# Optimization experiments

Measured on AMD Instinct MI355X. Metric: run time of the kernel, lower is better.

Reference implementation:

```python
import jax, jax.numpy as jnp
import numpy as np

D_MODEL = 1024
NUM_HEADS = 16
D_K = D_MODEL // NUM_HEADS


def setup_inputs() -> dict:
    key = jax.random.key(0)
    ks = jax.random.split(key, 10)
    s = 1.0 / np.sqrt(D_MODEL)  # ~ torch Linear init scale
    inp = {
        "x": jax.random.normal(ks[0], (2, 2048, D_MODEL), dtype=jnp.float32),
        "Wq": jax.random.uniform(ks[1], (D_MODEL, D_MODEL), jnp.float32, -s, s),
        "bq": jax.random.uniform(ks[2], (D_MODEL,), jnp.float32, -s, s),
        "Wk": jax.random.uniform(ks[3], (D_MODEL, D_MODEL), jnp.float32, -s, s),
        "bk": jax.random.uniform(ks[4], (D_MODEL,), jnp.float32, -s, s),
        "Wv": jax.random.uniform(ks[5], (D_MODEL, D_MODEL), jnp.float32, -s, s),
        "bv": jax.random.uniform(ks[6], (D_MODEL,), jnp.float32, -s, s),
        "Wo": jax.random.uniform(ks[7], (D_MODEL, D_MODEL), jnp.float32, -s, s),
        "bo": jax.random.uniform(ks[8], (D_MODEL,), jnp.float32, -s, s),
        "ln_gamma": jnp.ones((D_MODEL,), jnp.float32),
        "ln_beta": jnp.zeros((D_MODEL,), jnp.float32),
    }
    return inp


def reference(x, Wq, bq, Wk, bk, Wv, bv, Wo, bo, ln_gamma, ln_beta):
    B, S, D = x.shape
    residual = x
    # LayerNorm (eps=1e-5 as torch default)
    mu = jnp.mean(x, axis=-1, keepdims=True)
    var = jnp.mean(jnp.square(x - mu), axis=-1, keepdims=True)
    xn = (x - mu) * jax.lax.rsqrt(var + 1e-5) * ln_gamma + ln_beta
    # QKV projections (torch Linear: y = x @ W^T + b) -> (B, H, S, d_k)
    def proj(W, b):
        return (xn @ W.T + b).reshape(B, S, NUM_HEADS, D_K).transpose(0, 2, 1, 3)
    Q, K, V = proj(Wq, bq), proj(Wk, bk), proj(Wv, bv)
    scores = jnp.einsum("bhqd,bhkd->bhqk", Q, K) / np.sqrt(D_K).astype(np.float32)
    attn = jax.nn.softmax(scores, axis=-1)  # (B, H, S, S); dropout is no-op (eval)
    context = jnp.einsum("bhqk,bhkd->bhqd", attn, V)
    context = context.transpose(0, 2, 1, 3).reshape(B, S, D)
    out = context @ Wo.T + bo
    return out + residual, attn.mean(axis=1)
```

## Files before the change

kernel.cpp:

```cpp
#include <hip/hip_runtime.h>
#include <stdint.h>
#include <stddef.h>

#define DEV static __device__ __forceinline__

typedef float f32x4 __attribute__((ext_vector_type(4)));
typedef float f32x16 __attribute__((ext_vector_type(16)));
typedef unsigned u32x4 __attribute__((ext_vector_type(4)));
typedef __bf16 bf16x8 __attribute__((ext_vector_type(8)));

DEV short f2bf(float f) {
  union { float f; unsigned u; } a; a.f = f;
  unsigned r = a.u + 0x7fffu + ((a.u >> 16) & 1u);
  return (short)(r >> 16);
}

DEV void gld_lds16(const void* g, void* lds) {
  __builtin_amdgcn_global_load_lds(
      (__attribute__((address_space(1))) void*)(void*)g,
      (__attribute__((address_space(3))) void*)lds, 16, 0, 0);
}

DEV f32x4 MFMA(bf16x8 a, bf16x8 b, f32x4 c) {
  return __builtin_amdgcn_mfma_f32_16x16x32_bf16(a, b, c, 0, 0, 0);
}
DEV f32x16 MFMA32(bf16x8 a, bf16x8 b, f32x16 c) {
  return __builtin_amdgcn_mfma_f32_32x32x16_bf16(a, b, c, 0, 0, 0);
}

DEV float ex2(float x) { return __builtin_amdgcn_exp2f(x); }

DEV unsigned cvtpk(float lo, float hi) {
  unsigned r;
  asm("v_cvt_pk_bf16_f32 %0, %1, %2" : "=v"(r) : "v"(lo), "v"(hi));
  return r;
}

DEV float xhalf_sum(float v) {
  float a = v, b = v;
  asm volatile("v_permlane32_swap_b32 %0, %1" : "+v"(a), "+v"(b));
  return a + b;
}

#define LOG2E 1.4426950408889634f


__global__ __launch_bounds__(256) void k_cvtw_ln(
    const float* __restrict__ w0, const float* __restrict__ w1,
    const float* __restrict__ w2, const float* __restrict__ w3,
    short* __restrict__ dst, const float* __restrict__ x,
    const float* __restrict__ g, const float* __restrict__ be,
    short* __restrict__ xn) {
  __shared__ float ps[4], pss[4];
  if (blockIdx.x < 4096) {
    int i = blockIdx.x * 256 + threadIdx.x;
    int sel = i >> 18;
    const float* src = sel == 0 ? w0 : sel == 1 ? w1 : sel == 2 ? w2 : w3;
    int off = (i & 0x3ffff) * 4;
    float4 v = *(const float4*)(src + off);
    short4 o4; o4.x = f2bf(v.x); o4.y = f2bf(v.y); o4.z = f2bf(v.z); o4.w = f2bf(v.w);
    *(short4*)(dst + (size_t)i * 4) = o4;
  } else {
    int row = blockIdx.x - 4096;
    int t = threadIdx.x;
    const float4* xr = (const float4*)(x + (size_t)row * 1024);
    float4 v = xr[t];
    float s = v.x + v.y + v.z + v.w;
    float ss = v.x * v.x + v.y * v.y + v.z * v.z + v.w * v.w;
#pragma unroll
    for (int o = 32; o; o >>= 1) { s += __shfl_down(s, o); ss += __shfl_down(ss, o); }
    int w = t >> 6, lane = t & 63;
    if (lane == 0) { ps[w] = s; pss[w] = ss; }
    __syncthreads();
    float st = ps[0] + ps[1] + ps[2] + ps[3];
    float sst = pss[0] + pss[1] + pss[2] + pss[3];
    float mean = st * (1.0f / 1024.0f);
    float var = sst * (1.0f / 1024.0f) - mean * mean;
    float rstd = rsqrtf(var + 1e-5f);
    float4 gv = ((const float4*)g)[t];
    float4 bv = ((const float4*)be)[t];
    short4 o4;
    o4.x = f2bf((v.x - mean) * rstd * gv.x + bv.x);
    o4.y = f2bf((v.y - mean) * rstd * gv.y + bv.y);
    o4.z = f2bf((v.z - mean) * rstd * gv.z + bv.z);
    o4.w = f2bf((v.w - mean) * rstd * gv.w + bv.w);
    ((short4*)(xn + (size_t)row * 1024))[t] = o4;
  }
}

__global__ __launch_bounds__(256) void k_gemm_qkv(
    const short* __restrict__ xn, const short* __restrict__ wbf,
    const float* __restrict__ bq, const float* __restrict__ bk,
    const float* __restrict__ bv, short* __restrict__ q_ws,
    short* __restrict__ k_ws, short* __restrict__ v_ws) {
  __shared__ __align__(16) short at[128 * 32];
  __shared__ __align__(16) short bt[128 * 32];
  int t = threadIdx.x, lane = t & 63, w = t >> 6;
  int wr = w >> 1, wc = w & 1;
  int z = blockIdx.z;
  int row0 = blockIdx.y * 128, col0 = blockIdx.x * 128;
  const short* A = xn + (size_t)row0 * 1024;
  const short* Bw = wbf + (size_t)z * (1024 * 1024) + (size_t)col0 * 1024;
  f32x4 acc[4][4];
#pragma unroll
  for (int m = 0; m < 4; m++)
#pragma unroll
    for (int n = 0; n < 4; n++) acc[m][n] = (f32x4)0.0f;

  for (int k0 = 0; k0 < 1024; k0 += 32) {
#pragma unroll
    for (int i = 0; i < 2; i++) {
      int c = t + i * 256;
      int r = c >> 2, cc = (c & 3) * 8;
      gld_lds16(A + (size_t)r * 1024 + k0 + cc, &at[c * 8]);
      gld_lds16(Bw + (size_t)r * 1024 + k0 + cc, &bt[c * 8]);
    }
    __syncthreads();
    bf16x8 af[4], bfr[4];
#pragma unroll
    for (int m = 0; m < 4; m++)
      af[m] = *(const bf16x8*)&at[(wr * 64 + m * 16 + (lane & 15)) * 32 + (lane >> 4) * 8];
#pragma unroll
    for (int n = 0; n < 4; n++)
      bfr[n] = *(const bf16x8*)&bt[(wc * 64 + n * 16 + (lane & 15)) * 32 + (lane >> 4) * 8];
#pragma unroll
    for (int m = 0; m < 4; m++)
#pragma unroll
      for (int n = 0; n < 4; n++) acc[m][n] = MFMA(af[m], bfr[n], acc[m][n]);
    __syncthreads();
  }
  const float* bias = z == 0 ? bq : z == 1 ? bk : bv;
  short* dst = z == 0 ? q_ws : z == 1 ? k_ws : v_ws;
  float scal = z == 0 ? (0.125f * LOG2E) : 1.0f;
#pragma unroll
  for (int m = 0; m < 4; m++)
#pragma unroll
    for (int n = 0; n < 4; n++)
#pragma unroll
      for (int r = 0; r < 4; r++) {
        int grow = row0 + wr * 64 + m * 16 + (lane >> 4) * 4 + r;
        int gcol = col0 + wc * 64 + n * 16 + (lane & 15);
        float val = (acc[m][n][r] + bias[gcol]) * scal;
        int bb = grow >> 11, s = grow & 2047, h = gcol >> 6, d = gcol & 63;
        dst[(((size_t)bb * 16 + h) * 2048 + s) * 64 + d] = f2bf(val);
      }
}

__global__ __launch_bounds__(256) void k_trv(const short* __restrict__ v_ws,
                                             short* __restrict__ vt_ws) {
  __shared__ short tile[64][65];
  int bh = blockIdx.y, s0 = blockIdx.x * 64;
  const short* src = v_ws + ((size_t)bh * 2048 + s0) * 64;
  int t = threadIdx.x;
#pragma unroll
  for (int i = 0; i < 4; i++) {
    int c = t + i * 256;
    int r = c >> 4, d4 = (c & 15) * 4;
    short4 v4 = *(const short4*)&src[r * 64 + d4];
    tile[d4 + 0][r] = v4.x; tile[d4 + 1][r] = v4.y;
    tile[d4 + 2][r] = v4.z; tile[d4 + 3][r] = v4.w;
  }
  __syncthreads();
#pragma unroll
  for (int i = 0; i < 4; i++) {
    int c = t + i * 256;
    int d = c >> 4, r4 = (c & 15) * 4;
    short4 o4;
    o4.x = tile[d][r4 + 0]; o4.y = tile[d][r4 + 1];
    o4.z = tile[d][r4 + 2]; o4.w = tile[d][r4 + 3];
    *(short4*)&vt_ws[((size_t)bh * 64 + d) * 2048 + s0 + r4] = o4;
  }
}

__global__ __launch_bounds__(256, 2) void k_attn1(
    const short* __restrict__ q_ws, const short* __restrict__ k_ws,
    const short* __restrict__ vt_ws, short* __restrict__ o_ws,
    float* __restrict__ l_ws) {
  __shared__ __align__(16) short k_lds[4][64 * 64];
  __shared__ __align__(16) short vt_lds[5][64 * 64];
  int t = threadIdx.x, lane = t & 63, w = t >> 6;
  int hi = lane >> 5, l31 = lane & 31;
  int flat = blockIdx.x + 16 * blockIdx.y + 256 * blockIdx.z;
  int mm = (flat & 7) * 64 + (flat >> 3);
  int qt = mm & 15, hd = (mm >> 4) & 15, b = mm >> 8;
  int bh = b * 16 + hd;
  int q0 = qt * 128;
  const short* qb = q_ws + (size_t)bh * (2048 * 64);
  const short* kb = k_ws + (size_t)bh * (2048 * 64);
  const short* vtb = vt_ws + (size_t)bh * (64 * 2048);
  int qg = q0 + w * 32 + l31;

  bf16x8 qf[4];
#pragma unroll
  for (int d4 = 0; d4 < 4; d4++)
    qf[d4] = *(const bf16x8*)&qb[(size_t)qg * 64 + d4 * 16 + hi * 8];
  asm volatile("s_waitcnt vmcnt(0)" ::: "memory");

  const short *kp0, *kp1, *vp0, *vp1;
  {
    int c = t, r = c >> 3, j = (c & 7) ^ (r & 7);
    kp0 = kb + (size_t)r * 64 + j * 8;
    vp0 = vtb + (size_t)r * 2048 + j * 8;
  }
  {
    int c = t + 256, r = c >> 3, j = (c & 7) ^ (r & 7);
    kp1 = kb + (size_t)r * 64 + j * 8;
    vp1 = vtb + (size_t)r * 2048 + j * 8;
  }

  int koff[8];
#pragma unroll
  for (int d4 = 0; d4 < 4; d4++) {
    int row0 = l31, row1 = 32 + l31;
    koff[2 * d4]     = row0 * 64 + (((d4 * 2 + hi) ^ (row0 & 7)) * 8);
    koff[2 * d4 + 1] = row1 * 64 + (((d4 * 2 + hi) ^ (row1 & 7)) * 8);
  }

#define STG(tl_)                                                         \
  {                                                                      \
    gld_lds16(kp0 + (size_t)(tl_) * 4096, &k_lds[(tl_) & 3][t * 8]);     \
    gld_lds16(kp1 + (size_t)(tl_) * 4096, &k_lds[(tl_) & 3][(t + 256) * 8]); \
    gld_lds16(vp0 + (size_t)(tl_) * 64, &vt_lds[(tl_) % 5][t * 8]);      \
    gld_lds16(vp1 + (size_t)(tl_) * 64, &vt_lds[(tl_) % 5][(t + 256) * 8]); \
  }

  STG(0);
  STG(1);

  f32x16 Oacc[2];
#pragma unroll
  for (int i = 0; i < 16; i++) { Oacc[0][i] = 0.0f; Oacc[1][i] = 0.0f; }
  float lrun = 0.0f;
  bf16x8 pb[4];

  for (int it = 0; it < 32; ++it) {
    int tn = it + 2 <= 31 ? it + 2 : 31;
    STG(tn);
    asm volatile("s_waitcnt vmcnt(8)" ::: "memory");
    __builtin_amdgcn_s_barrier();

    const short* kl = k_lds[it & 3];
    const short* vl = vt_lds[(it + 4) % 5];

    bf16x8 kfr[8], vfr[8];
#pragma unroll
    for (int i = 0; i < 8; i++) kfr[i] = *(const bf16x8*)&kl[koff[i]];
#pragma unroll
    for (int i = 0; i < 8; i++) vfr[i] = *(const bf16x8*)&vl[koff[i]];

    __builtin_amdgcn_s_setprio(1);
    f32x16 S0 = (f32x16)0.0f, S1 = (f32x16)0.0f;
#pragma unroll
    for (int d4 = 0; d4 < 4; d4++) {
      S0 = MFMA32(kfr[2 * d4], qf[d4], S0);
      S1 = MFMA32(kfr[2 * d4 + 1], qf[d4], S1);
    }
    if (it) {
#pragma unroll
      for (int ks = 0; ks < 4; ks++) {
        Oacc[0] = MFMA32(vfr[2 * ks], pb[ks], Oacc[0]);
        Oacc[1] = MFMA32(vfr[2 * ks + 1], pb[ks], Oacc[1]);
      }
    }
    __builtin_amdgcn_s_setprio(0);

    float rs0 = 0.0f, rs1 = 0.0f;
#pragma unroll
    for (int i = 0; i < 16; i++) {
      float p0 = ex2(S0[i]);
      float p1 = ex2(S1[i]);
      S0[i] = p0; S1[i] = p1;
      rs0 += p0; rs1 += p1;
    }
    lrun += xhalf_sum(rs0 + rs1);

#pragma unroll
    for (int ks = 0; ks < 4; ks++) {
      unsigned wA, wB, wC, wD;
      if (ks == 0) {
        wA = cvtpk(S0[0], S0[1]);  wB = cvtpk(S0[2], S0[3]);
        wC = cvtpk(S0[4], S0[5]);  wD = cvtpk(S0[6], S0[7]);
      } else if (ks == 1) {
        wA = cvtpk(S0[8], S0[9]);  wB = cvtpk(S0[10], S0[11]);
        wC = cvtpk(S0[12], S0[13]); wD = cvtpk(S0[14], S0[15]);
      } else if (ks == 2) {
        wA = cvtpk(S1[0], S1[1]);  wB = cvtpk(S1[2], S1[3]);
        wC = cvtpk(S1[4], S1[5]);  wD = cvtpk(S1[6], S1[7]);
      } else {
        wA = cvtpk(S1[8], S1[9]);  wB = cvtpk(S1[10], S1[11]);
        wC = cvtpk(S1[12], S1[13]); wD = cvtpk(S1[14], S1[15]);
      }
      asm volatile("v_permlane32_swap_b32 %0, %1" : "+v"(wA), "+v"(wC));
      asm volatile("v_permlane32_swap_b32 %0, %1" : "+v"(wB), "+v"(wD));
      u32x4 uu; uu.x = wA; uu.y = wB; uu.z = wC; uu.w = wD;
      pb[ks] = __builtin_bit_cast(bf16x8, uu);
    }
  }
  asm volatile("s_waitcnt vmcnt(0)" ::: "memory");
  __builtin_amdgcn_s_barrier();

  {
    const short* vl = vt_lds[1];
    __builtin_amdgcn_s_setprio(1);
#pragma unroll
    for (int ks = 0; ks < 4; ks++) {
      Oacc[0] = MFMA32(*(const bf16x8*)&vl[koff[2 * ks]], pb[ks], Oacc[0]);
      Oacc[1] = MFMA32(*(const bf16x8*)&vl[koff[2 * ks + 1]], pb[ks], Oacc[1]);
    }
    __builtin_amdgcn_s_setprio(0);
  }

  float rl = 1.0f / lrun;
  if (lane < 32) {
    l_ws[bh * 2048 + qg] = rl;
  }
#pragma unroll
  for (int dt = 0; dt < 2; dt++)
#pragma unroll
    for (int g = 0; g < 4; g++) {
      short4 o4;
      o4.x = f2bf(Oacc[dt][g * 4 + 0] * rl);
      o4.y = f2bf(Oacc[dt][g * 4 + 1] * rl);
      o4.z = f2bf(Oacc[dt][g * 4 + 2] * rl);
      o4.w = f2bf(Oacc[dt][g * 4 + 3] * rl);
      int d = dt * 32 + g * 8 + hi * 4;
      *(short4*)&o_ws[((size_t)(b * 2048 + qg)) * 1024 + hd * 64 + d] = o4;
    }
}

__global__ __launch_bounds__(256, 3) void k_attn2(
    const short* __restrict__ q_ws, const short* __restrict__ k_ws,
    const float* __restrict__ l_ws, float* __restrict__ out1) {
  __shared__ __align__(16) short k_lds2[3][128 * 64];
  __shared__ __align__(16) float l_lds[3][64];
  int t = threadIdx.x, lane = t & 63, w = t >> 6;
  int flat = blockIdx.x + 16 * blockIdx.y + 512 * blockIdx.z;
  int mm = (flat & 7) * 128 + (flat >> 3);
  int q0 = (mm & 31) * 64, k2 = ((mm >> 5) & 15) * 128, b = mm >> 9;

  f32x4 pacc[8];
#pragma unroll
  for (int n = 0; n < 8; n++) pacc[n] = (f32x4)0.0f;

  int qrow = q0 + w * 16 + (lane & 15);
  size_t qoff0 = (size_t)qrow * 64 + (lane >> 4) * 8;
  const short* qb0 = q_ws + (size_t)(b * 16) * (2048 * 64);

#define STAGE2(hh)                                                               \
  {                                                                              \
    int bh_ = b * 16 + (hh);                                                     \
    const short* kb_ = k_ws + (size_t)bh_ * (2048 * 64);                         \
    _Pragma("unroll")                                                            \
    for (int i = 0; i < 4; i++) {                                                \
      int c = t + i * 256;                                                       \
      int r = c >> 3, j = (c & 7) ^ (r & 7);                                     \
      gld_lds16(kb_ + (size_t)(k2 + r) * 64 + j * 8, &k_lds2[(hh) % 3][c * 8]);  \
    }                                                                            \
    int cc = w * 4 + (t & 63);                                                   \
    if ((t & 63) < 4) {                                                          \
      gld_lds16(&l_ws[(size_t)bh_ * 2048 + q0 + cc * 4], &l_lds[(hh) % 3][cc * 4]); \
    }                                                                            \
  }

  STAGE2(0);
  for (int h = 0; h < 16; ++h) {
    bf16x8 qf0 = *(const bf16x8*)&qb0[(size_t)h * (2048 * 64) + qoff0];
    bf16x8 qf1 = *(const bf16x8*)&qb0[(size_t)h * (2048 * 64) + qoff0 + 32];
    int hn = h < 15 ? h + 1 : 15;
    STAGE2(hn);
    asm volatile("s_waitcnt vmcnt(5)" ::: "memory");
    __builtin_amdgcn_s_barrier();

    const short* kl = k_lds2[h % 3];
    f32x4 sc[8];
#pragma unroll
    for (int n = 0; n < 8; n++) sc[n] = (f32x4)0.0f;
#pragma unroll
    for (int kf = 0; kf < 2; kf++)
#pragma unroll
      for (int n = 0; n < 8; n++) {
        int row = n * 16 + (lane & 15);
        bf16x8 kfr = *(const bf16x8*)&kl[row * 64 + (((kf * 4 + (lane >> 4)) ^ (row & 7)) * 8)];
        sc[n] = MFMA(kf == 0 ? qf0 : qf1, kfr, sc[n]);
      }
    f32x4 lh = *(const f32x4*)&l_lds[h % 3][w * 16 + (lane >> 4) * 4];
#pragma unroll
    for (int n = 0; n < 8; n++)
#pragma unroll
      for (int r = 0; r < 4; r++)
        pacc[n][r] += ex2(sc[n][r]) * lh[r];
  }

#pragma unroll
  for (int n = 0; n < 8; n++)
#pragma unroll
    for (int r = 0; r < 4; r++) {
      int q = q0 + w * 16 + (lane >> 4) * 4 + r;
      int k = k2 + n * 16 + (lane & 15);
      out1[((size_t)b * 2048 + q) * 2048 + k] = pacc[n][r] * 0.0625f;
    }
}

__global__ __launch_bounds__(256) void k_gemm_out(
    const short* __restrict__ o_ws, const short* __restrict__ wo_bf,
    const float* __restrict__ bo, const float* __restrict__ x,
    float* __restrict__ out0) {
  __shared__ __align__(16) short at[128 * 32];
  __shared__ __align__(16) short bt[128 * 32];
  int t = threadIdx.x, lane = t & 63, w = t >> 6;
  int wr = w >> 1, wc = w & 1;
  int row0 = blockIdx.y * 128, col0 = blockIdx.x * 128;
  const short* A = o_ws + (size_t)row0 * 1024;
  const short* Bw = wo_bf + (size_t)col0 * 1024;
  f32x4 acc[4][4];
#pragma unroll
  for (int m = 0; m < 4; m++)
#pragma unroll
    for (int n = 0; n < 4; n++) acc[m][n] = (f32x4)0.0f;

  for (int k0 = 0; k0 < 1024; k0 += 32) {
#pragma unroll
    for (int i = 0; i < 2; i++) {
      int c = t + i * 256;
      int r = c >> 2, cc = (c & 3) * 8;
      gld_lds16(A + (size_t)r * 1024 + k0 + cc, &at[c * 8]);
      gld_lds16(Bw + (size_t)r * 1024 + k0 + cc, &bt[c * 8]);
    }
    __syncthreads();
    bf16x8 af[4], bfr[4];
#pragma unroll
    for (int m = 0; m < 4; m++)
      af[m] = *(const bf16x8*)&at[(wr * 64 + m * 16 + (lane & 15)) * 32 + (lane >> 4) * 8];
#pragma unroll
    for (int n = 0; n < 4; n++)
      bfr[n] = *(const bf16x8*)&bt[(wc * 64 + n * 16 + (lane & 15)) * 32 + (lane >> 4) * 8];
#pragma unroll
    for (int m = 0; m < 4; m++)
#pragma unroll
      for (int n = 0; n < 4; n++) acc[m][n] = MFMA(af[m], bfr[n], acc[m][n]);
    __syncthreads();
  }
#pragma unroll
  for (int m = 0; m < 4; m++)
#pragma unroll
    for (int n = 0; n < 4; n++)
#pragma unroll
      for (int r = 0; r < 4; r++) {
        int grow = row0 + wr * 64 + m * 16 + (lane >> 4) * 4 + r;
        int gcol = col0 + wc * 64 + n * 16 + (lane & 15);
        float val = acc[m][n][r] + bo[gcol] + x[(size_t)grow * 1024 + gcol];
        out0[(size_t)grow * 1024 + gcol] = val;
      }
}

extern "C" void kernel_launch(void* const* d_in, const int* in_sizes, int n_in,
                              void* d_out, int out_size, void* d_ws, size_t ws_size,
                              hipStream_t stream) {
  (void)in_sizes; (void)n_in; (void)out_size; (void)ws_size;
  const float* x   = (const float*)d_in[0];
  const float* Wq  = (const float*)d_in[1];
  const float* bq  = (const float*)d_in[2];
  const float* Wk  = (const float*)d_in[3];
  const float* bk  = (const float*)d_in[4];
  const float* Wv  = (const float*)d_in[5];
  const float* bv  = (const float*)d_in[6];
  const float* Wo  = (const float*)d_in[7];
  const float* bo  = (const float*)d_in[8];
  const float* lng = (const float*)d_in[9];
  const float* lnb = (const float*)d_in[10];
  float* out0 = (float*)d_out;
  float* out1 = out0 + (size_t)2 * 2048 * 1024;

  char* ws = (char*)d_ws;
  short* xn    = (short*)(ws);
  short* q_ws  = (short*)(ws + 8388608);
  short* k_ws  = (short*)(ws + 16777216);
  short* o_ws  = (short*)(ws + 25165824);
  short* vt_ws = (short*)(ws + 33554432);
  short* wbf   = (short*)(ws + 41943040);
  float* l_ws  = (float*)(ws + 50331648);

  k_cvtw_ln<<<8192, 256, 0, stream>>>(Wq, Wk, Wv, Wo, wbf, x, lng, lnb, xn);
  k_gemm_qkv<<<dim3(8, 32, 3), 256, 0, stream>>>(xn, wbf, bq, bk, bv, q_ws, k_ws, o_ws);
  k_trv<<<dim3(32, 32), 256, 0, stream>>>(o_ws, vt_ws);
  k_attn1<<<dim3(16, 16, 2), 256, 0, stream>>>(q_ws, k_ws, vt_ws, o_ws, l_ws);
  k_attn2<<<dim3(16, 32, 2), 256, 0, stream>>>(q_ws, k_ws, l_ws, out1);
  k_gemm_out<<<dim3(8, 32), 256, 0, stream>>>(o_ws, wbf + (size_t)3 * 1024 * 1024, bo, x, out0);
}
```

Measured before the change: 161.8 us.

## Merge attention-map and output-projection kernels into one heterogeneous launch

Combines k_attn2 (averaged attention probabilities) and k_gemm_out (output projection plus residual) into a single kernel, k_tail, that dispatches on blockIdx: the first 256 blocks run the GEMM and the remaining 1024 run the attention-map pass. This removes one launch and the serialization gap between the two independent kernels, letting their work overlap on the GPU. In exchange the shared LDS allocation becomes the larger of the two and the launch_bounds occupancy hint of 3 is dropped, which may lower occupancy for the attention-map blocks.

Result: no change. 161.0 us (-0.5%).

```diff
diff --git a/kernel.cpp b/kernel.cpp
--- a/kernel.cpp
+++ b/kernel.cpp
@@ -328,129 +328,133 @@
     }
 }
 
-__global__ __launch_bounds__(256, 3) void k_attn2(
+__global__ __launch_bounds__(256) void k_tail(
     const short* __restrict__ q_ws, const short* __restrict__ k_ws,
-    const float* __restrict__ l_ws, float* __restrict__ out1) {
-  __shared__ __align__(16) short k_lds2[3][128 * 64];
-  __shared__ __align__(16) float l_lds[3][64];
-  int t = threadIdx.x, lane = t & 63, w = t >> 6;
-  int flat = blockIdx.x + 16 * blockIdx.y + 512 * blockIdx.z;
-  int mm = (flat & 7) * 128 + (flat >> 3);
-  int q0 = (mm & 31) * 64, k2 = ((mm >> 5) & 15) * 128, b = mm >> 9;
-
-  f32x4 pacc[8];
-#pragma unroll
-  for (int n = 0; n < 8; n++) pacc[n] = (f32x4)0.0f;
-
-  int qrow = q0 + w * 16 + (lane & 15);
-  size_t qoff0 = (size_t)qrow * 64 + (lane >> 4) * 8;
-  const short* qb0 = q_ws + (size_t)(b * 16) * (2048 * 64);
-
-#define STAGE2(hh)                                                               \
-  {                                                                              \
-    int bh_ = b * 16 + (hh);                                                     \
-    const short* kb_ = k_ws + (size_t)bh_ * (2048 * 64);                         \
-    _Pragma("unroll")                                                            \
-    for (int i = 0; i < 4; i++) {                                                \
-      int c = t + i * 256;                                                       \
-      int r = c >> 3, j = (c & 7) ^ (r & 7);                                     \
-      gld_lds16(kb_ + (size_t)(k2 + r) * 64 + j * 8, &k_lds2[(hh) % 3][c * 8]);  \
-    }                                                                            \
-    int cc = w * 4 + (t & 63);                                                   \
-    if ((t & 63) < 4) {                                                          \
-      gld_lds16(&l_ws[(size_t)bh_ * 2048 + q0 + cc * 4], &l_lds[(hh) % 3][cc * 4]); \
-    }                                                                            \
-  }
-
-  STAGE2(0);
-  for (int h = 0; h < 16; ++h) {
-    bf16x8 qf0 = *(const bf16x8*)&qb0[(size_t)h * (2048 * 64) + qoff0];
-    bf16x8 qf1 = *(const bf16x8*)&qb0[(size_t)h * (2048 * 64) + qoff0 + 32];
-    int hn = h < 15 ? h + 1 : 15;
-    STAGE2(hn);
-    asm volatile("s_waitcnt vmcnt(5)" ::: "memory");
-    __builtin_amdgcn_s_barrier();
-
-    const short* kl = k_lds2[h % 3];
-    f32x4 sc[8];
-#pragma unroll
-    for (int n = 0; n < 8; n++) sc[n] = (f32x4)0.0f;
-#pragma unroll
-    for (int kf = 0; kf < 2; kf++)
-#pragma unroll
-      for (int n = 0; n < 8; n++) {
-        int row = n * 16 + (lane & 15);
-        bf16x8 kfr = *(const bf16x8*)&kl[row * 64 + (((kf * 4 + (lane >> 4)) ^ (row & 7)) * 8)];
-        sc[n] = MFMA(kf == 0 ? qf0 : qf1, kfr, sc[n]);
-      }
-    f32x4 lh = *(const f32x4*)&l_lds[h % 3][w * 16 + (lane >> 4) * 4];
-#pragma unroll
-    for (int n = 0; n < 8; n++)
-#pragma unroll
-      for (int r = 0; r < 4; r++)
-        pacc[n][r] += ex2(sc[n][r]) * lh[r];
-  }
-
-#pragma unroll
-  for (int n = 0; n < 8; n++)
-#pragma unroll
-    for (int r = 0; r < 4; r++) {
-      int q = q0 + w * 16 + (lane >> 4) * 4 + r;
-      int k = k2 + n * 16 + (lane & 15);
-      out1[((size_t)b * 2048 + q) * 2048 + k] = pacc[n][r] * 0.0625f;
-    }
-}
-
-__global__ __launch_bounds__(256) void k_gemm_out(
+    const float* __restrict__ l_ws, float* __restrict__ out1,
     const short* __restrict__ o_ws, const short* __restrict__ wo_bf,
     const float* __restrict__ bo, const float* __restrict__ x,
     float* __restrict__ out0) {
-  __shared__ __align__(16) short at[128 * 32];
-  __shared__ __align__(16) short bt[128 * 32];
+  __shared__ __align__(16) char smem[3 * 16384 + 3 * 256];
   int t = threadIdx.x, lane = t & 63, w = t >> 6;
-  int wr = w >> 1, wc = w & 1;
-  int row0 = blockIdx.y * 128, col0 = blockIdx.x * 128;
-  const short* A = o_ws + (size_t)row0 * 1024;
-  const short* Bw = wo_bf + (size_t)col0 * 1024;
-  f32x4 acc[4][4];
-#pragma unroll
-  for (int m = 0; m < 4; m++)
-#pragma unroll
-    for (int n = 0; n < 4; n++) acc[m][n] = (f32x4)0.0f;
-
-  for (int k0 = 0; k0 < 1024; k0 += 32) {
-#pragma unroll
-    for (int i = 0; i < 2; i++) {
-      int c = t + i * 256;
-      int r = c >> 2, cc = (c & 3) * 8;
-      gld_lds16(A + (size_t)r * 1024 + k0 + cc, &at[c * 8]);
-      gld_lds16(Bw + (size_t)r * 1024 + k0 + cc, &bt[c * 8]);
-    }
-    __syncthreads();
-    bf16x8 af[4], bfr[4];
+
+  if (blockIdx.x < 256) {
+    short* at = (short*)smem;
+    short* bt = (short*)(smem + 8192);
+    int wr = w >> 1, wc = w & 1;
+    int fo = blockIdx.x;
+    int col0 = (fo & 7) * 128, row0 = (fo >> 3) * 128;
+    const short* A = o_ws + (size_t)row0 * 1024;
+    const short* Bw = wo_bf + (size_t)col0 * 1024;
+    f32x4 acc[4][4];
 #pragma unroll
     for (int m = 0; m < 4; m++)
-      af[m] = *(const bf16x8*)&at[(wr * 64 + m * 16 + (lane & 15)) * 32 + (lane >> 4) * 8];
-#pragma unroll
-    for (int n = 0; n < 4; n++)
-      bfr[n] = *(const bf16x8*)&bt[(wc * 64 + n * 16 + (lane & 15)) * 32 + (lane >> 4) * 8];
+#pragma unroll
+      for (int n = 0; n < 4; n++) acc[m][n] = (f32x4)0.0f;
+
+    for (int k0 = 0; k0 < 1024; k0 += 32) {
+#pragma unroll
+      for (int i = 0; i < 2; i++) {
+        int c = t + i * 256;
+        int r = c >> 2, cc = (c & 3) * 8;
+        gld_lds16(A + (size_t)r * 1024 + k0 + cc, &at[c * 8]);
+        gld_lds16(Bw + (size_t)r * 1024 + k0 + cc, &bt[c * 8]);
+      }
+      __syncthreads();
+      bf16x8 af[4], bfr[4];
+#pragma unroll
+      for (int m = 0; m < 4; m++)
+        af[m] = *(const bf16x8*)&at[(wr * 64 + m * 16 + (lane & 15)) * 32 + (lane >> 4) * 8];
+#pragma unroll
+      for (int n = 0; n < 4; n++)
+        bfr[n] = *(const bf16x8*)&bt[(wc * 64 + n * 16 + (lane & 15)) * 32 + (lane >> 4) * 8];
+#pragma unroll
+      for (int m = 0; m < 4; m++)
+#pragma unroll
+        for (int n = 0; n < 4; n++) acc[m][n] = MFMA(af[m], bfr[n], acc[m][n]);
+      __syncthreads();
+    }
 #pragma unroll
     for (int m = 0; m < 4; m++)
 #pragma unroll
-      for (int n = 0; n < 4; n++) acc[m][n] = MFMA(af[m], bfr[n], acc[m][n]);
-    __syncthreads();
-  }
-#pragma unroll
-  for (int m = 0; m < 4; m++)
-#pragma unroll
-    for (int n = 0; n < 4; n++)
+      for (int n = 0; n < 4; n++)
+#pragma unroll
+        for (int r = 0; r < 4; r++) {
+          int grow = row0 + wr * 64 + m * 16 + (lane >> 4) * 4 + r;
+          int gcol = col0 + wc * 64 + n * 16 + (lane & 15);
+          float val = acc[m][n][r] + bo[gcol] + x[(size_t)grow * 1024 + gcol];
+          out0[(size_t)grow * 1024 + gcol] = val;
+        }
+  } else {
+    short* k_lds2 = (short*)smem;
+    float* l_lds = (float*)(smem + 49152);
+    int flat = blockIdx.x - 256;
+    int mm = (flat & 7) * 128 + (flat >> 3);
+    int q0 = (mm & 31) * 64, k2 = ((mm >> 5) & 15) * 128, b = mm >> 9;
+
+    f32x4 pacc[8];
+#pragma unroll
+    for (int n = 0; n < 8; n++) pacc[n] = (f32x4)0.0f;
+
+    int qrow = q0 + w * 16 + (lane & 15);
+    size_t qoff0 = (size_t)qrow * 64 + (lane >> 4) * 8;
+    const short* qb0 = q_ws + (size_t)(b * 16) * (2048 * 64);
+
+#define STAGE2(hh)                                                               \
+    {                                                                            \
+      int bh_ = b * 16 + (hh);                                                   \
+      const short* kb_ = k_ws + (size_t)bh_ * (2048 * 64);                       \
+      short* kdst_ = k_lds2 + ((hh) % 3) * (128 * 64);                           \
+      _Pragma("unroll")                                                          \
+      for (int i = 0; i < 4; i++) {                                              \
+        int c = t + i * 256;                                                     \
+        int r = c >> 3, j = (c & 7) ^ (r & 7);                                   \
+        gld_lds16(kb_ + (size_t)(k2 + r) * 64 + j * 8, &kdst_[c * 8]);           \
+      }                                                                          \
+      int cc = w * 4 + (t & 63);                                                 \
+      if ((t & 63) < 4) {                                                        \
+        gld_lds16(&l_ws[(size_t)bh_ * 2048 + q0 + cc * 4],                       \
+                  &l_lds[((hh) % 3) * 64 + cc * 4]);                             \
+      }                                                                          \
+    }
+
+    STAGE2(0);
+    for (int h = 0; h < 16; ++h) {
+      bf16x8 qf0 = *(const bf16x8*)&qb0[(size_t)h * (2048 * 64) + qoff0];
+      bf16x8 qf1 = *(const bf16x8*)&qb0[(size_t)h * (2048 * 64) + qoff0 + 32];
+      int hn = h < 15 ? h + 1 : 15;
+      STAGE2(hn);
+      asm volatile("s_waitcnt vmcnt(5)" ::: "memory");
+      __builtin_amdgcn_s_barrier();
+
+      const short* kl = k_lds2 + (h % 3) * (128 * 64);
+      f32x4 sc[8];
+#pragma unroll
+      for (int n = 0; n < 8; n++) sc[n] = (f32x4)0.0f;
+#pragma unroll
+      for (int kf = 0; kf < 2; kf++)
+#pragma unroll
+        for (int n = 0; n < 8; n++) {
+          int row = n * 16 + (lane & 15);
+          bf16x8 kfr = *(const bf16x8*)&kl[row * 64 + (((kf * 4 + (lane >> 4)) ^ (row & 7)) * 8)];
+          sc[n] = MFMA(kf == 0 ? qf0 : qf1, kfr, sc[n]);
+        }
+      f32x4 lh = *(const f32x4*)&l_lds[(h % 3) * 64 + w * 16 + (lane >> 4) * 4];
+#pragma unroll
+      for (int n = 0; n < 8; n++)
+#pragma unroll
+        for (int r = 0; r < 4; r++)
+          pacc[n][r] += ex2(sc[n][r]) * lh[r];
+    }
+
+#pragma unroll
+    for (int n = 0; n < 8; n++)
 #pragma unroll
       for (int r = 0; r < 4; r++) {
-        int grow = row0 + wr * 64 + m * 16 + (lane >> 4) * 4 + r;
-        int gcol = col0 + wc * 64 + n * 16 + (lane & 15);
-        float val = acc[m][n][r] + bo[gcol] + x[(size_t)grow * 1024 + gcol];
-        out0[(size_t)grow * 1024 + gcol] = val;
+        int q = q0 + w * 16 + (lane >> 4) * 4 + r;
+        int k = k2 + n * 16 + (lane & 15);
+        out1[((size_t)b * 2048 + q) * 2048 + k] = pacc[n][r] * 0.0625f;
       }
+  }
 }
 
 extern "C" void kernel_launch(void* const* d_in, const int* in_sizes, int n_in,
@@ -484,6 +488,6 @@
   k_gemm_qkv<<<dim3(8, 32, 3), 256, 0, stream>>>(xn, wbf, bq, bk, bv, q_ws, k_ws, o_ws);
   k_trv<<<dim3(32, 32), 256, 0, stream>>>(o_ws, vt_ws);
   k_attn1<<<dim3(16, 16, 2), 256, 0, stream>>>(q_ws, k_ws, vt_ws, o_ws, l_ws);
-  k_attn2<<<dim3(16, 32, 2), 256, 0, stream>>>(q_ws, k_ws, l_ws, out1);
-  k_gemm_out<<<dim3(8, 32), 256, 0, stream>>>(o_ws, wbf + (size_t)3 * 1024 * 1024, bo, x, out0);
-}
+  k_tail<<<1280, 256, 0, stream>>>(q_ws, k_ws, l_ws, out1,
+                                   o_ws, wbf + (size_t)3 * 1024 * 1024, bo, x, out0);
+}
```
